# Kernel tuning notes

Measured on AMD Instinct MI355X. Metric: run time of the kernel, lower is better.

## Reference

```python
import jax, jax.numpy as jnp
import numpy as np

B, T, I, H = 64, 2048, 64, 128


def setup_inputs() -> dict:
    key = jax.random.key(0)
    ks = jax.random.split(key, 6)
    std = 1.0 / np.sqrt(H)
    return {
        "x": jax.random.normal(ks[0], (B, T, I), dtype=jnp.float32),
        "h0": jax.random.normal(ks[1], (B, H), dtype=jnp.float32),
        "W": jax.random.uniform(ks[2], (H, I), dtype=jnp.float32, minval=-std, maxval=std),
        "U": jax.random.uniform(ks[3], (H, H), dtype=jnp.float32, minval=-std, maxval=std),
        "b_ih": jax.random.uniform(ks[4], (H,), dtype=jnp.float32, minval=-std, maxval=std),
        "b_hh": jax.random.uniform(ks[5], (H,), dtype=jnp.float32, minval=-std, maxval=std),
    }


def reference(x, h0, W, U, b_ih, b_hh):
    # Precompute the input projection for all timesteps in one big GEMM:
    # xw[b,t,h] = W x_t + b_ih + b_hh  (biases folded in once)
    xw = jnp.einsum("bti,hi->bth", x, W) + b_ih + b_hh  # [B,T,H]
    xw_t = jnp.swapaxes(xw, 0, 1)  # [T,B,H] for scan over time

    def step(h, xt):
        # vanilla tanh RNN cell: h' = tanh(W x + U h + b_ih + b_hh)
        h_new = jnp.tanh(xt + h @ U.T)
        return h_new, h_new

    h_last, ys = jax.lax.scan(step, h0, xw_t)  # ys: [T,B,H]
    output = jnp.swapaxes(ys, 0, 1)  # batch_first -> [B,T,H]
    return output, h_last
```

## Files before the change

### kernel.cpp

```cpp
#include <hip/hip_runtime.h>


#define RNN_B 64
#define RNN_T 2048
#define RNN_I 64
#define RNN_H 128
#define CH    32
#define NCH   (RNN_T / CH)

__device__ __forceinline__ float fast_tanh(float x) {
  float e = __builtin_amdgcn_exp2f(x * 2.885390081777927f);
  return 1.0f - 2.0f * __builtin_amdgcn_rcpf(e + 1.0f);
}

template <int CTRL>
__device__ __forceinline__ float dpp_add(float s) {
  int o = __builtin_amdgcn_mov_dpp(__float_as_int(s), CTRL, 0xF, 0xF, true);
  return s + __int_as_float(o);
}

__device__ __forceinline__ void fma4(float4& a, const float4 u, const float4 h) {
  a.x = fmaf(u.x, h.x, a.x);
  a.y = fmaf(u.y, h.y, a.y);
  a.z = fmaf(u.z, h.z, a.z);
  a.w = fmaf(u.w, h.w, a.w);
}

__device__ __forceinline__ float hsum(const float4 a) {
  return (a.x + a.y) + (a.z + a.w);
}

__device__ __forceinline__ void barrier_lgkm() {
  asm volatile("s_waitcnt lgkmcnt(0)\n\ts_barrier" ::: "memory");
}

__global__ __launch_bounds__(256, 2) void rnn_xw_gemm(
    const float* __restrict__ x, const float* __restrict__ W,
    const float* __restrict__ b_ih, const float* __restrict__ b_hh,
    float* __restrict__ xw) {
  const int tid = threadIdx.x;
  const int g   = tid >> 2;
  const int q   = tid & 3;

  float4 w[2][4];
#pragma unroll
  for (int r = 0; r < 2; ++r) {
    const float4* Wr = (const float4*)(W + (2 * g + r) * RNN_I + 16 * q);
#pragma unroll
    for (int m = 0; m < 4; ++m) w[r][m] = Wr[m];
  }
  const int row_own = 2 * g + (q & 1);
  const float bias  = b_ih[row_own] + b_hh[row_own];

  __shared__ __align__(16) float4 xs[64 * 16];
  const long rbase = (long)blockIdx.x * 64;
  const float4* xg = (const float4*)(x + rbase * RNN_I);
#pragma unroll
  for (int jj = 0; jj < 4; ++jj) xs[tid + 256 * jj] = xg[tid + 256 * jj];
  __syncthreads();

#pragma unroll 4
  for (int r = 0; r < 64; ++r) {
    const float4* xr = xs + r * 16 + q * 4;
    float4 a0 = {0, 0, 0, 0}, a1 = {0, 0, 0, 0};
#pragma unroll
    for (int m = 0; m < 4; ++m) {
      const float4 xv = xr[m];
      fma4(a0, w[0][m], xv);
      fma4(a1, w[1][m], xv);
    }
    float s0 = hsum(a0), s1 = hsum(a1);
    s0 = dpp_add<0xB1>(s0); s0 = dpp_add<0x4E>(s0);
    s1 = dpp_add<0xB1>(s1); s1 = dpp_add<0x4E>(s1);
    const float own = (q & 1) ? s1 : s0;
    if (q < 2)
      xw[(rbase + r) * RNN_H + row_own] = own + bias;
  }
}

__global__ __launch_bounds__(512, 2) void rnn_scan(
    const float* xw,
    float* out, float* __restrict__ hlast,
    const float* __restrict__ h0, const float* __restrict__ U) {
  const int b     = blockIdx.x;
  const int tid   = threadIdx.x;
  const int g     = tid >> 3;
  const int j     = tid & 7;
  const int r_own = 2 * g + (j & 1);

  __shared__ __align__(16) float hbuf0[8 * 20];
  __shared__ __align__(16) float hbuf1[8 * 20];
  __shared__ __align__(16) float xbuf[CH * RNN_H];
  __shared__ __align__(16) float obuf[CH * RNN_H];

  float4 u[2][4];
#pragma unroll
  for (int r = 0; r < 2; ++r) {
    const float4* Ur = (const float4*)(U + (2 * g + r) * RNN_H + 16 * j);
#pragma unroll
    for (int m = 0; m < 4; ++m) u[r][m] = Ur[m];
  }

  if (tid < RNN_H)
    hbuf0[(tid >> 4) * 20 + (tid & 15)] = h0[b * RNN_H + tid];

  const int hoff = (r_own >> 4) * 20 + (r_own & 15);
  const long base   = (long)b * RNN_T * RNN_H;
  const float4* xw4 = (const float4*)(xw + base);
  float4* out4      = (float4*)(out + base);
  float4* xb4       = (float4*)xbuf;
  const float4* ob4 = (const float4*)obuf;

  float4 p0 = xw4[tid], p1 = xw4[tid + 512];

  float xv_cur;

  auto step = [&](const float* src, float* dst, int tc) {
    const float4* hp = (const float4*)(src + 20 * j);
    float4 a0 = {0, 0, 0, 0}, a1 = {0, 0, 0, 0};
#pragma unroll
    for (int m = 0; m < 4; ++m) {
      const float4 hv = hp[m];
      fma4(a0, u[0][m], hv);
      fma4(a1, u[1][m], hv);
    }
    const float xv_next = xbuf[((tc + 1) & (CH - 1)) * RNN_H + r_own];
    float s0 = hsum(a0), s1 = hsum(a1);
    s0 = dpp_add<0xB1>(s0); s0 = dpp_add<0x4E>(s0); s0 = dpp_add<0x141>(s0);
    s1 = dpp_add<0xB1>(s1); s1 = dpp_add<0x4E>(s1); s1 = dpp_add<0x141>(s1);
    const float own = (j & 1) ? s1 : s0;
    const float val = fast_tanh(own + xv_cur);
    if (j < 2) {
      dst[hoff] = val;
    } else if ((j & 6) == 4) {
      obuf[tc * RNN_H + r_own] = val;
    }
    barrier_lgkm();
    xv_cur = xv_next;
  };

  for (int c = 0; c < NCH; ++c) {
    xb4[tid] = p0; xb4[tid + 512] = p1;
    if (c + 1 < NCH) {
      const float4* nx = xw4 + (long)(c + 1) * 1024;
      p0 = nx[tid]; p1 = nx[tid + 512];
    }
    if (c > 0) {
      out4[(long)(c - 1) * 1024 + tid]       = ob4[tid];
      out4[(long)(c - 1) * 1024 + tid + 512] = ob4[tid + 512];
    }
    barrier_lgkm();

    xv_cur = xbuf[r_own];
    for (int tc = 0; tc < CH; tc += 2) {
      step(hbuf0, hbuf1, tc);
      step(hbuf1, hbuf0, tc + 1);
    }
  }

  out4[(long)(NCH - 1) * 1024 + tid]       = ob4[tid];
  out4[(long)(NCH - 1) * 1024 + tid + 512] = ob4[tid + 512];
  if (tid < RNN_H)
    hlast[b * RNN_H + tid] = hbuf0[(tid >> 4) * 20 + (tid & 15)];
}

extern "C" void kernel_launch(void* const* d_in, const int* in_sizes, int n_in,
                              void* d_out, int out_size, void* d_ws, size_t ws_size,
                              hipStream_t stream) {
  const float* x    = (const float*)d_in[0];
  const float* h0   = (const float*)d_in[1];
  const float* W    = (const float*)d_in[2];
  const float* U    = (const float*)d_in[3];
  const float* b_ih = (const float*)d_in[4];
  const float* b_hh = (const float*)d_in[5];

  float* out   = (float*)d_out;
  float* hlast = out + (long)RNN_B * RNN_T * RNN_H;

  rnn_xw_gemm<<<(RNN_B * RNN_T) / 64, 256, 0, stream>>>(x, W, b_ih, b_hh, out);
  rnn_scan<<<RNN_B, 512, 0, stream>>>(out, out, hlast, h0, U);
}
```

Baseline: 661.5 us.

## Process two batch rows per scan block and prefetch GEMM x rows

The scan kernel now handles two independent batch sequences per workgroup (32 blocks instead of 64). It interleaves their matvec, reduction and tanh work so each per-step barrier and its latency are amortized over twice the independent arithmetic. Chunk size is halved so shared memory stays bounded. The xw GEMM kernel also software-prefetches the next x row from LDS into registers. The trade-off is that only 32 CUs run the latency-bound scan, so it depends on per-step latency hiding rather than breadth across the device.

```diff
diff --git a/kernel.cpp b/kernel.cpp
--- a/kernel.cpp
+++ b/kernel.cpp
@@ -5,7 +5,7 @@
 #define RNN_T 2048
 #define RNN_I 64
 #define RNN_H 128
-#define CH    32
+#define CH    16
 #define NCH   (RNN_T / CH)
 
 __device__ __forceinline__ float fast_tanh(float x) {
@@ -59,16 +59,18 @@
   for (int jj = 0; jj < 4; ++jj) xs[tid + 256 * jj] = xg[tid + 256 * jj];
   __syncthreads();
 
+  const float4* xr0 = xs + q * 4;
+  float4 n0 = xr0[0], n1 = xr0[1], n2 = xr0[2], n3 = xr0[3];
 #pragma unroll 4
   for (int r = 0; r < 64; ++r) {
-    const float4* xr = xs + r * 16 + q * 4;
+    const float4 hv0 = n0, hv1 = n1, hv2 = n2, hv3 = n3;
+    const float4* xn = xs + ((r + 1) & 63) * 16 + q * 4;
+    n0 = xn[0]; n1 = xn[1]; n2 = xn[2]; n3 = xn[3];
     float4 a0 = {0, 0, 0, 0}, a1 = {0, 0, 0, 0};
-#pragma unroll
-    for (int m = 0; m < 4; ++m) {
-      const float4 xv = xr[m];
-      fma4(a0, w[0][m], xv);
-      fma4(a1, w[1][m], xv);
-    }
+    fma4(a0, w[0][0], hv0); fma4(a0, w[0][1], hv1);
+    fma4(a0, w[0][2], hv2); fma4(a0, w[0][3], hv3);
+    fma4(a1, w[1][0], hv0); fma4(a1, w[1][1], hv1);
+    fma4(a1, w[1][2], hv2); fma4(a1, w[1][3], hv3);
     float s0 = hsum(a0), s1 = hsum(a1);
     s0 = dpp_add<0xB1>(s0); s0 = dpp_add<0x4E>(s0);
     s1 = dpp_add<0xB1>(s1); s1 = dpp_add<0x4E>(s1);
@@ -78,20 +80,20 @@
   }
 }
 
-__global__ __launch_bounds__(512, 2) void rnn_scan(
+__global__ __launch_bounds__(512, 1) void rnn_scan(
     const float* xw,
     float* out, float* __restrict__ hlast,
     const float* __restrict__ h0, const float* __restrict__ U) {
-  const int b     = blockIdx.x;
-  const int tid   = threadIdx.x;
-  const int g     = tid >> 3;
-  const int j     = tid & 7;
+  const int bp  = blockIdx.x;
+  const int tid = threadIdx.x;
+  const int g   = tid >> 3;
+  const int j   = tid & 7;
   const int r_own = 2 * g + (j & 1);
 
-  __shared__ __align__(16) float hbuf0[8 * 20];
-  __shared__ __align__(16) float hbuf1[8 * 20];
-  __shared__ __align__(16) float xbuf[CH * RNN_H];
-  __shared__ __align__(16) float obuf[CH * RNN_H];
+  __shared__ __align__(16) float hb0[2][160];
+  __shared__ __align__(16) float hb1[2][160];
+  __shared__ __align__(16) float xbuf[2][CH * RNN_H];
+  __shared__ __align__(16) float obuf[2][CH * RNN_H];
 
   float4 u[2][4];
 #pragma unroll
@@ -101,67 +103,94 @@
     for (int m = 0; m < 4; ++m) u[r][m] = Ur[m];
   }
 
-  if (tid < RNN_H)
-    hbuf0[(tid >> 4) * 20 + (tid & 15)] = h0[b * RNN_H + tid];
+  if (tid < RNN_H) {
+    hb0[0][(tid >> 4) * 20 + (tid & 15)] = h0[(2 * bp) * RNN_H + tid];
+  } else if (tid < 2 * RNN_H) {
+    const int t = tid - RNN_H;
+    hb0[1][(t >> 4) * 20 + (t & 15)] = h0[(2 * bp + 1) * RNN_H + t];
+  }
 
   const int hoff = (r_own >> 4) * 20 + (r_own & 15);
-  const long base   = (long)b * RNN_T * RNN_H;
-  const float4* xw4 = (const float4*)(xw + base);
-  float4* out4      = (float4*)(out + base);
-  float4* xb4       = (float4*)xbuf;
-  const float4* ob4 = (const float4*)obuf;
-
-  float4 p0 = xw4[tid], p1 = xw4[tid + 512];
-
-  float xv_cur;
-
-  auto step = [&](const float* src, float* dst, int tc) {
-    const float4* hp = (const float4*)(src + 20 * j);
-    float4 a0 = {0, 0, 0, 0}, a1 = {0, 0, 0, 0};
-#pragma unroll
-    for (int m = 0; m < 4; ++m) {
-      const float4 hv = hp[m];
-      fma4(a0, u[0][m], hv);
-      fma4(a1, u[1][m], hv);
-    }
-    const float xv_next = xbuf[((tc + 1) & (CH - 1)) * RNN_H + r_own];
-    float s0 = hsum(a0), s1 = hsum(a1);
-    s0 = dpp_add<0xB1>(s0); s0 = dpp_add<0x4E>(s0); s0 = dpp_add<0x141>(s0);
-    s1 = dpp_add<0xB1>(s1); s1 = dpp_add<0x4E>(s1); s1 = dpp_add<0x141>(s1);
-    const float own = (j & 1) ? s1 : s0;
-    const float val = fast_tanh(own + xv_cur);
+  const long base0   = (long)(2 * bp) * RNN_T * RNN_H;
+  const long base1   = (long)(2 * bp + 1) * RNN_T * RNN_H;
+  const float4* xw40 = (const float4*)(xw + base0);
+  const float4* xw41 = (const float4*)(xw + base1);
+  float4* out40      = (float4*)(out + base0);
+  float4* out41      = (float4*)(out + base1);
+  float4* xb40       = (float4*)xbuf[0];
+  float4* xb41       = (float4*)xbuf[1];
+  const float4* ob40 = (const float4*)obuf[0];
+  const float4* ob41 = (const float4*)obuf[1];
+
+  float4 p0 = xw40[tid], p1 = xw41[tid];
+
+  float xv0, xv1;
+
+  auto step = [&](const float* sA, const float* sB, float* dA, float* dB,
+                  int tc) {
+    const float4* hpA = (const float4*)(sA + 20 * j);
+    const float4* hpB = (const float4*)(sB + 20 * j);
+    const float4 A0 = hpA[0], A1 = hpA[1], A2 = hpA[2], A3 = hpA[3];
+    const float4 B0 = hpB[0], B1 = hpB[1], B2 = hpB[2], B3 = hpB[3];
+    float4 a0 = {0,0,0,0}, a1 = {0,0,0,0};
+    float4 c0 = {0,0,0,0}, c1 = {0,0,0,0};
+    fma4(a0, u[0][0], A0); fma4(a0, u[0][1], A1);
+    fma4(a0, u[0][2], A2); fma4(a0, u[0][3], A3);
+    fma4(a1, u[1][0], A0); fma4(a1, u[1][1], A1);
+    fma4(a1, u[1][2], A2); fma4(a1, u[1][3], A3);
+    fma4(c0, u[0][0], B0); fma4(c0, u[0][1], B1);
+    fma4(c0, u[0][2], B2); fma4(c0, u[0][3], B3);
+    fma4(c1, u[1][0], B0); fma4(c1, u[1][1], B1);
+    fma4(c1, u[1][2], B2); fma4(c1, u[1][3], B3);
+    const float xn0 = xbuf[0][((tc + 1) & (CH - 1)) * RNN_H + r_own];
+    const float xn1 = xbuf[1][((tc + 1) & (CH - 1)) * RNN_H + r_own];
+    float sa0 = hsum(a0), sa1 = hsum(a1), sc0 = hsum(c0), sc1 = hsum(c1);
+    sa0 = dpp_add<0xB1>(sa0); sa0 = dpp_add<0x4E>(sa0); sa0 = dpp_add<0x141>(sa0);
+    sa1 = dpp_add<0xB1>(sa1); sa1 = dpp_add<0x4E>(sa1); sa1 = dpp_add<0x141>(sa1);
+    sc0 = dpp_add<0xB1>(sc0); sc0 = dpp_add<0x4E>(sc0); sc0 = dpp_add<0x141>(sc0);
+    sc1 = dpp_add<0xB1>(sc1); sc1 = dpp_add<0x4E>(sc1); sc1 = dpp_add<0x141>(sc1);
+    const float ownA = (j & 1) ? sa1 : sa0;
+    const float ownB = (j & 1) ? sc1 : sc0;
+    const float vA = fast_tanh(ownA + xv0);
+    const float vB = fast_tanh(ownB + xv1);
     if (j < 2) {
-      dst[hoff] = val;
+      dA[hoff] = vA;
+      dB[hoff] = vB;
     } else if ((j & 6) == 4) {
-      obuf[tc * RNN_H + r_own] = val;
+      obuf[0][tc * RNN_H + r_own] = vA;
+      obuf[1][tc * RNN_H + r_own] = vB;
     }
     barrier_lgkm();
-    xv_cur = xv_next;
+    xv0 = xn0; xv1 = xn1;
   };
 
   for (int c = 0; c < NCH; ++c) {
-    xb4[tid] = p0; xb4[tid + 512] = p1;
+    xb40[tid] = p0; xb41[tid] = p1;
     if (c + 1 < NCH) {
-      const float4* nx = xw4 + (long)(c + 1) * 1024;
-      p0 = nx[tid]; p1 = nx[tid + 512];
+      p0 = xw40[(long)(c + 1) * 512 + tid];
+      p1 = xw41[(long)(c + 1) * 512 + tid];
     }
     if (c > 0) {
-      out4[(long)(c - 1) * 1024 + tid]       = ob4[tid];
-      out4[(long)(c - 1) * 1024 + tid + 512] = ob4[tid + 512];
+      out40[(long)(c - 1) * 512 + tid] = ob40[tid];
+      out41[(long)(c - 1) * 512 + tid] = ob41[tid];
     }
     barrier_lgkm();
 
-    xv_cur = xbuf[r_own];
+    xv0 = xbuf[0][r_own]; xv1 = xbuf[1][r_own];
     for (int tc = 0; tc < CH; tc += 2) {
-      step(hbuf0, hbuf1, tc);
-      step(hbuf1, hbuf0, tc + 1);
-    }
-  }
-
-  out4[(long)(NCH - 1) * 1024 + tid]       = ob4[tid];
-  out4[(long)(NCH - 1) * 1024 + tid + 512] = ob4[tid + 512];
-  if (tid < RNN_H)
-    hlast[b * RNN_H + tid] = hbuf0[(tid >> 4) * 20 + (tid & 15)];
+      step(hb0[0], hb0[1], hb1[0], hb1[1], tc);
+      step(hb1[0], hb1[1], hb0[0], hb0[1], tc + 1);
+    }
+  }
+
+  out40[(long)(NCH - 1) * 512 + tid] = ob40[tid];
+  out41[(long)(NCH - 1) * 512 + tid] = ob41[tid];
+  if (tid < RNN_H) {
+    hlast[(2 * bp) * RNN_H + tid] = hb0[0][(tid >> 4) * 20 + (tid & 15)];
+  } else if (tid < 2 * RNN_H) {
+    const int t = tid - RNN_H;
+    hlast[(2 * bp + 1) * RNN_H + t] = hb0[1][(t >> 4) * 20 + (t & 15)];
+  }
 }
 
 extern "C" void kernel_launch(void* const* d_in, const int* in_sizes, int n_in,
@@ -178,5 +207,5 @@
   float* hlast = out + (long)RNN_B * RNN_T * RNN_H;
 
   rnn_xw_gemm<<<(RNN_B * RNN_T) / 64, 256, 0, stream>>>(x, W, b_ih, b_hh, out);
-  rnn_scan<<<RNN_B, 512, 0, stream>>>(out, out, hlast, h0, U);
-}
+  rnn_scan<<<RNN_B / 2, 512, 0, stream>>>(out, out, hlast, h0, U);
+}
```

After: 977.5 us. 1.48x slower.

## Use inline-asm LDS reads for h and x, drop chunk prefetch registers

Applied to the files above, without the earlier changes.

Replaces the compiler-generated LDS float4 loads in both the GEMM and the scan step with an inline-asm block that issues four ds_read_b128 and waits once, so the read pattern is fixed. The scan no longer prefetches the next chunk of xw into registers during the current chunk. Instead it loads the current chunk at the start of each chunk, which exposes global load latency once per chunk in exchange for lower register pressure. The GEMM unroll is also lowered from 4 to 2.

```diff
diff --git a/kernel.cpp b/kernel.cpp
--- a/kernel.cpp
+++ b/kernel.cpp
@@ -7,6 +7,8 @@
 #define RNN_H 128
 #define CH    32
 #define NCH   (RNN_T / CH)
+
+typedef float v4f __attribute__((ext_vector_type(4)));
 
 __device__ __forceinline__ float fast_tanh(float x) {
   float e = __builtin_amdgcn_exp2f(x * 2.885390081777927f);
@@ -19,7 +21,7 @@
   return s + __int_as_float(o);
 }
 
-__device__ __forceinline__ void fma4(float4& a, const float4 u, const float4 h) {
+__device__ __forceinline__ void fma4v(float4& a, const float4 u, const v4f h) {
   a.x = fmaf(u.x, h.x, a.x);
   a.y = fmaf(u.y, h.y, a.y);
   a.z = fmaf(u.z, h.z, a.z);
@@ -28,6 +30,22 @@
 
 __device__ __forceinline__ float hsum(const float4 a) {
   return (a.x + a.y) + (a.z + a.w);
+}
+
+__device__ __forceinline__ unsigned lds_off(const void* p) {
+  return (unsigned)(unsigned long long)p;
+}
+
+__device__ __forceinline__ void ds_read4(unsigned base, v4f& r0, v4f& r1,
+                                         v4f& r2, v4f& r3) {
+  asm volatile(
+      "ds_read_b128 %0, %4\n\t"
+      "ds_read_b128 %1, %4 offset:16\n\t"
+      "ds_read_b128 %2, %4 offset:32\n\t"
+      "ds_read_b128 %3, %4 offset:48\n\t"
+      "s_waitcnt lgkmcnt(0)"
+      : "=&v"(r0), "=&v"(r1), "=&v"(r2), "=&v"(r3)
+      : "v"(base));
 }
 
 __device__ __forceinline__ void barrier_lgkm() {
@@ -59,16 +77,15 @@
   for (int jj = 0; jj < 4; ++jj) xs[tid + 256 * jj] = xg[tid + 256 * jj];
   __syncthreads();
 
-#pragma unroll 4
+#pragma unroll 2
   for (int r = 0; r < 64; ++r) {
-    const float4* xr = xs + r * 16 + q * 4;
+    v4f hv0, hv1, hv2, hv3;
+    ds_read4(lds_off(xs + r * 16 + q * 4), hv0, hv1, hv2, hv3);
     float4 a0 = {0, 0, 0, 0}, a1 = {0, 0, 0, 0};
-#pragma unroll
-    for (int m = 0; m < 4; ++m) {
-      const float4 xv = xr[m];
-      fma4(a0, w[0][m], xv);
-      fma4(a1, w[1][m], xv);
-    }
+    fma4v(a0, w[0][0], hv0); fma4v(a0, w[0][1], hv1);
+    fma4v(a0, w[0][2], hv2); fma4v(a0, w[0][3], hv3);
+    fma4v(a1, w[1][0], hv0); fma4v(a1, w[1][1], hv1);
+    fma4v(a1, w[1][2], hv2); fma4v(a1, w[1][3], hv3);
     float s0 = hsum(a0), s1 = hsum(a1);
     s0 = dpp_add<0xB1>(s0); s0 = dpp_add<0x4E>(s0);
     s1 = dpp_add<0xB1>(s1); s1 = dpp_add<0x4E>(s1);
@@ -105,26 +122,25 @@
     hbuf0[(tid >> 4) * 20 + (tid & 15)] = h0[b * RNN_H + tid];
 
   const int hoff = (r_own >> 4) * 20 + (r_own & 15);
+  const unsigned hb0 = lds_off(hbuf0 + 20 * j);
+  const unsigned hb1 = lds_off(hbuf1 + 20 * j);
   const long base   = (long)b * RNN_T * RNN_H;
   const float4* xw4 = (const float4*)(xw + base);
   float4* out4      = (float4*)(out + base);
   float4* xb4       = (float4*)xbuf;
   const float4* ob4 = (const float4*)obuf;
 
-  float4 p0 = xw4[tid], p1 = xw4[tid + 512];
-
   float xv_cur;
 
-  auto step = [&](const float* src, float* dst, int tc) {
-    const float4* hp = (const float4*)(src + 20 * j);
+  auto step = [&](unsigned hb, float* dst, int tc) {
+    v4f hv0, hv1, hv2, hv3;
+    ds_read4(hb, hv0, hv1, hv2, hv3);
+    float xv_next = xbuf[((tc + 1) & (CH - 1)) * RNN_H + r_own];
     float4 a0 = {0, 0, 0, 0}, a1 = {0, 0, 0, 0};
-#pragma unroll
-    for (int m = 0; m < 4; ++m) {
-      const float4 hv = hp[m];
-      fma4(a0, u[0][m], hv);
-      fma4(a1, u[1][m], hv);
-    }
-    const float xv_next = xbuf[((tc + 1) & (CH - 1)) * RNN_H + r_own];
+    fma4v(a0, u[0][0], hv0); fma4v(a0, u[0][1], hv1);
+    fma4v(a0, u[0][2], hv2); fma4v(a0, u[0][3], hv3);
+    fma4v(a1, u[1][0], hv0); fma4v(a1, u[1][1], hv1);
+    fma4v(a1, u[1][2], hv2); fma4v(a1, u[1][3], hv3);
     float s0 = hsum(a0), s1 = hsum(a1);
     s0 = dpp_add<0xB1>(s0); s0 = dpp_add<0x4E>(s0); s0 = dpp_add<0x141>(s0);
     s1 = dpp_add<0xB1>(s1); s1 = dpp_add<0x4E>(s1); s1 = dpp_add<0x141>(s1);
@@ -140,21 +156,19 @@
   };
 
   for (int c = 0; c < NCH; ++c) {
-    xb4[tid] = p0; xb4[tid + 512] = p1;
-    if (c + 1 < NCH) {
-      const float4* nx = xw4 + (long)(c + 1) * 1024;
-      p0 = nx[tid]; p1 = nx[tid + 512];
-    }
+    const float4* nx = xw4 + (long)c * 1024;
+    float4 t0 = nx[tid], t1 = nx[tid + 512];
     if (c > 0) {
       out4[(long)(c - 1) * 1024 + tid]       = ob4[tid];
       out4[(long)(c - 1) * 1024 + tid + 512] = ob4[tid + 512];
     }
+    xb4[tid] = t0; xb4[tid + 512] = t1;
     barrier_lgkm();
 
     xv_cur = xbuf[r_own];
     for (int tc = 0; tc < CH; tc += 2) {
-      step(hbuf0, hbuf1, tc);
-      step(hbuf1, hbuf0, tc + 1);
+      step(hb0, hbuf1, tc);
+      step(hb1, hbuf0, tc + 1);
     }
   }
 
```

New measurement: 728.4 us. 10.1% more time.
